# Performance work log

Hardware: AMD Instinct MI355X
Metric: run time of the kernel (lower is better)

## Reference

```python
import jax, jax.numpy as jnp
import numpy as np

L = 8          # fixed number of instance labels (0 = background), all assumed present
DV = 0.5       # delta_v
DD = 1.5       # delta_d
LOSS_WEIGHT = 1.0


def _safe_norm(x, axis):
    sq = jnp.sum(x * x, axis=axis)
    pos = sq > 0
    return jnp.sqrt(jnp.where(pos, sq, 1.0)) * pos.astype(x.dtype)


def _per_image(emb, inst, kern, tmask):
    # emb: [D,H,W], inst: [H,W] int, kern/tmask: [H,W] float
    D, H, W = emb.shape
    HW = H * W
    tm = (tmask > 0.5).astype(inst.dtype)
    kb = (kern > 0.5).astype(inst.dtype)
    inst = inst * tm
    inst_k = (inst * kb).reshape(-1)          # kernel-region labels
    inst_f = inst.reshape(-1)                 # full-region labels
    emb_f = emb.reshape(D, -1).T              # [HW, D]

    # --- generate_coef: first/second occurrence (row-major) of each label ---
    flat = jnp.arange(HW)
    eq = inst_f[None, :] == jnp.arange(L)[:, None]          # [L, HW]
    idxs = jnp.where(eq, flat[None, :], HW)
    first = jnp.min(idxs, axis=1)
    second = jnp.min(jnp.where(idxs == first[:, None], HW, idxs), axis=1)
    first = jnp.minimum(first, HW - 1)
    second = jnp.minimum(second, HW - 1)
    r0, c0 = first // W, first % W
    r1, c1 = second // W, second % W
    # pos_id = (tmp[0,0], tmp[1,0], tmp[0,-1], tmp[1,-1]) as in the source
    pos = jnp.stack([r0, r1, c0, c1], axis=1).astype(jnp.float32)  # [L,4]
    diag = jnp.sqrt(jnp.float32(H * H + W * W))
    coef_diag = jnp.exp(jnp.sqrt((pos[:, 0] - pos[:, 2]) ** 2 +
                                 (pos[:, 1] - pos[:, 3]) ** 2) / diag / 2.0)
    zmask = (jnp.arange(L) > 0).astype(jnp.float32)          # skip label 0
    coef_diag = coef_diag * zmask
    s = pos[:, 0] + pos[:, 2]
    t = pos[:, 1] + pos[:, 3]
    dp = jnp.sqrt((s[:, None] - s[None, :]) ** 2 + (t[:, None] - t[None, :]) ** 2)
    coef_off = 1.0 - 20.0 * jnp.exp(-4.0 - 2.5 * dp / diag)
    eye = jnp.eye(L, dtype=bool)
    coef = jnp.where(eye, coef_diag[:, None], coef_off)
    coef = coef * zmask[:, None] * zmask[None, :]

    # --- per-label kernel means (segment mean) ---
    ones = jnp.ones((HW,), jnp.float32)
    cnt_k = jax.ops.segment_sum(ones, inst_k, num_segments=L)
    mean = jax.ops.segment_sum(emb_f, inst_k, num_segments=L)
    mean = mean / jnp.maximum(cnt_k, 1.0)[:, None]           # [L, D]
    mean = mean * zmask[:, None]

    # --- l_agg: per-pixel distance to own-label mean, segment-mean per label ---
    mean_px = mean[inst_f]                                   # [HW, D] gather
    dist = _safe_norm(emb_f - mean_px, axis=1)
    cd_px = coef_diag[inst_f]
    val = jnp.log(jax.nn.relu(cd_px * dist - DV) ** 2 + 1.0)
    cnt = jax.ops.segment_sum(ones, inst_f, num_segments=L)
    l_agg_per = jax.ops.segment_sum(val, inst_f, num_segments=L) / jnp.maximum(cnt, 1.0)
    l_agg = jnp.mean(l_agg_per[1:])

    # --- l_dis: coefficient-weighted pairwise hinge between means ---
    Dn = _safe_norm(mean[:, None, :] - mean[None, :, :], axis=-1)  # [L, L]
    pm = (~eye) & (zmask[:, None] > 0) & (zmask[None, :] > 0)
    vals = jnp.log(jax.nn.relu(2.0 * DD - coef * Dn) ** 2 + 1.0)
    l_dis = jnp.sum(jnp.where(pm, vals, 0.0)) / ((L - 1) * (L - 2))

    # --- l_reg ---
    l_reg = jnp.mean(jnp.log(_safe_norm(mean, axis=1) + 1.0)) * 0.001
    return l_agg + l_dis + l_reg


def reference(emb, instance, kernel, training_mask, bboxes):
    # bboxes is accepted but unused, matching the original forward_single
    loss_batch = jax.vmap(_per_image)(emb, instance, kernel, training_mask)
    return LOSS_WEIGHT * jnp.mean(loss_batch)


def setup_inputs() -> dict:
    key = jax.random.key(0)
    k1, k2, k3, k4, k5 = jax.random.split(key, 5)
    B, D, H, W = 8, 4, 640, 640
    emb = jax.random.normal(k1, (B, D, H, W), dtype=jnp.float32)
    instance = jax.random.randint(k2, (B, H, W), 0, L, dtype=jnp.int32)
    kernel = jax.random.uniform(k3, (B, H, W), dtype=jnp.float32)
    training_mask = jax.random.uniform(k4, (B, H, W), dtype=jnp.float32)
    bboxes = jax.random.uniform(k5, (B, 10, 4), dtype=jnp.float32)
    return {"emb": emb, "instance": instance, "kernel": kernel,
            "training_mask": training_mask, "bboxes": bboxes}
```

## Files before the change

### kernel.cpp

```cpp
#include <hip/hip_runtime.h>
#include <hip/hip_bf16.h>

#define B_   8
#define D_   4
#define H_   640
#define W_   640
#define HW_  (H_ * W_)
#define L_   8
#define BLOCK 256
#define ITER  8


__device__ __forceinline__ void fatom_add(float* p, float v) {
    unsafeAtomicAdd(p, v);
}

__global__ void k_init(int* firstIdx, int* secondIdx, float* fbuf) {
    int t = threadIdx.x;
    if (t < B_ * L_) { firstIdx[t] = HW_; secondIdx[t] = HW_; }
    for (int i = t; i < 448; i += blockDim.x) fbuf[i] = 0.0f;
}

__global__ __launch_bounds__(BLOCK) void k_pass1(
        const float* __restrict__ emb, const int* __restrict__ inst,
        const float* __restrict__ kern, const float* __restrict__ tmask,
        int* __restrict__ firstIdx, float* __restrict__ cntk,
        float* __restrict__ cntf, float* __restrict__ sumemb) {
    __shared__ int   sFirst[L_];
    __shared__ float sCntK[L_], sCntF[L_];
    __shared__ float sSum[L_ * D_];

    const int tid = threadIdx.x;
    if (tid < L_) { sFirst[tid] = HW_; sCntK[tid] = 0.0f; sCntF[tid] = 0.0f; }
    if (tid < L_ * D_) sSum[tid] = 0.0f;
    __syncthreads();

    const int b    = blockIdx.y;
    const int base = b * HW_;

    #pragma unroll
    for (int it = 0; it < ITER; ++it) {
        int p = blockIdx.x * (BLOCK * ITER) + it * BLOCK + tid;
        int lab  = inst[base + p];
        float tm = tmask[base + p];
        int lf = (tm > 0.5f) ? lab : 0;
        if (lf > 0) {
            atomicMin(&sFirst[lf], p);
            fatom_add(&sCntF[lf], 1.0f);
            float kn = kern[base + p];
            if (kn > 0.5f) {
                fatom_add(&sCntK[lf], 1.0f);
                #pragma unroll
                for (int d = 0; d < D_; ++d)
                    fatom_add(&sSum[lf * D_ + d], emb[(b * D_ + d) * HW_ + p]);
            }
        }
    }
    __syncthreads();

    if (tid >= 1 && tid < L_) {
        atomicMin(&firstIdx[b * L_ + tid], sFirst[tid]);
        fatom_add(&cntf[b * L_ + tid], sCntF[tid]);
        fatom_add(&cntk[b * L_ + tid], sCntK[tid]);
    }
    if (tid >= D_ && tid < L_ * D_)
        fatom_add(&sumemb[b * L_ * D_ + tid], sSum[tid]);
}

__global__ __launch_bounds__(BLOCK) void k_pass2(
        const int* __restrict__ inst, const float* __restrict__ tmask,
        const int* __restrict__ firstIdx, int* __restrict__ secondIdx) {
    __shared__ int sFirst[L_];
    __shared__ int sSecond[L_];

    const int tid = threadIdx.x;
    const int b   = blockIdx.y;
    if (tid < L_) { sFirst[tid] = firstIdx[b * L_ + tid]; sSecond[tid] = HW_; }
    __syncthreads();

    const int base = b * HW_;
    #pragma unroll
    for (int it = 0; it < ITER; ++it) {
        int p = blockIdx.x * (BLOCK * ITER) + it * BLOCK + tid;
        int lab  = inst[base + p];
        float tm = tmask[base + p];
        int lf = (tm > 0.5f) ? lab : 0;
        if (lf > 0 && p != sFirst[lf]) atomicMin(&sSecond[lf], p);
    }
    __syncthreads();

    if (tid >= 1 && tid < L_)
        atomicMin(&secondIdx[b * L_ + tid], sSecond[tid]);
}

__global__ __launch_bounds__(BLOCK) void k_pass3(
        const float* __restrict__ emb, const int* __restrict__ inst,
        const float* __restrict__ tmask,
        const int* __restrict__ firstIdx, const int* __restrict__ secondIdx,
        const float* __restrict__ cntk, const float* __restrict__ sumemb,
        float* __restrict__ sumval) {
    __shared__ float sMean[L_ * D_];
    __shared__ float sCd[L_];
    __shared__ float sVal[L_];

    const int tid = threadIdx.x;
    const int b   = blockIdx.y;

    if (tid < L_ * D_) {
        int l = tid / D_;
        float c = fmaxf(cntk[b * L_ + l], 1.0f);
        sMean[tid] = (l > 0) ? sumemb[b * L_ * D_ + tid] / c : 0.0f;
    }
    if (tid < L_) {
        float cd = 0.0f;
        if (tid > 0) {
            const float diag = sqrtf((float)(H_ * H_ + W_ * W_));
            int f = min(firstIdx[b * L_ + tid],  HW_ - 1);
            int s = min(secondIdx[b * L_ + tid], HW_ - 1);
            float r0 = (float)(f / W_), c0 = (float)(f % W_);
            float r1 = (float)(s / W_), c1 = (float)(s % W_);
            cd = expf(sqrtf((r0 - c0) * (r0 - c0) + (r1 - c1) * (r1 - c1))
                      / diag * 0.5f);
        }
        sCd[tid]  = cd;
        sVal[tid] = 0.0f;
    }
    __syncthreads();

    const int base = b * HW_;
    #pragma unroll
    for (int it = 0; it < ITER; ++it) {
        int p = blockIdx.x * (BLOCK * ITER) + it * BLOCK + tid;
        int lab  = inst[base + p];
        float tm = tmask[base + p];
        int lf = (tm > 0.5f) ? lab : 0;
        if (lf > 0) {
            float d2 = 0.0f;
            #pragma unroll
            for (int d = 0; d < D_; ++d) {
                float e = emb[(b * D_ + d) * HW_ + p] - sMean[lf * D_ + d];
                d2 += e * e;
            }
            float dist = (d2 > 0.0f) ? sqrtf(d2) : 0.0f;
            float x = sCd[lf] * dist - 0.5f;
            if (x > 0.0f) fatom_add(&sVal[lf], logf(x * x + 1.0f));
        }
    }
    __syncthreads();

    if (tid >= 1 && tid < L_)
        fatom_add(&sumval[b * L_ + tid], sVal[tid]);
}

__global__ void k_final(const int* __restrict__ firstIdx,
                        const int* __restrict__ secondIdx,
                        const float* __restrict__ cntk,
                        const float* __restrict__ cntf,
                        const float* __restrict__ sumemb,
                        const float* __restrict__ sumval,
                        float* __restrict__ out) {
    __shared__ float sLoss[B_];
    const int b = threadIdx.x;
    if (b < B_) {
        const float diag = sqrtf((float)(H_ * H_ + W_ * W_));
        float mean[L_][D_];
        float ss[L_], tt[L_];
        #pragma unroll
        for (int l = 0; l < L_; ++l) {
            float c = fmaxf(cntk[b * L_ + l], 1.0f);
            #pragma unroll
            for (int d = 0; d < D_; ++d)
                mean[l][d] = (l > 0) ? sumemb[(b * L_ + l) * D_ + d] / c : 0.0f;
            int f = min(firstIdx[b * L_ + l],  HW_ - 1);
            int s = min(secondIdx[b * L_ + l], HW_ - 1);
            float r0 = (float)(f / W_), c0 = (float)(f % W_);
            float r1 = (float)(s / W_), c1 = (float)(s % W_);
            ss[l] = r0 + c0;
            tt[l] = r1 + c1;
        }
        float ldis = 0.0f;
        #pragma unroll
        for (int i = 1; i < L_; ++i) {
            #pragma unroll
            for (int j = 1; j < L_; ++j) {
                if (i == j) continue;
                float d2 = 0.0f;
                #pragma unroll
                for (int d = 0; d < D_; ++d) {
                    float df = mean[i][d] - mean[j][d];
                    d2 += df * df;
                }
                float Dn = (d2 > 0.0f) ? sqrtf(d2) : 0.0f;
                float dx = ss[i] - ss[j], dy = tt[i] - tt[j];
                float dp = sqrtf(dx * dx + dy * dy);
                float coef = 1.0f - 20.0f * expf(-4.0f - 2.5f * dp / diag);
                float x = 3.0f - coef * Dn;
                if (x > 0.0f) ldis += logf(x * x + 1.0f);
            }
        }
        ldis *= (1.0f / 42.0f);
        float lreg = 0.0f;
        #pragma unroll
        for (int l = 0; l < L_; ++l) {
            float d2 = 0.0f;
            #pragma unroll
            for (int d = 0; d < D_; ++d) d2 += mean[l][d] * mean[l][d];
            float n = (d2 > 0.0f) ? sqrtf(d2) : 0.0f;
            lreg += logf(n + 1.0f);
        }
        lreg = lreg * (1.0f / L_) * 0.001f;
        float lagg = 0.0f;
        #pragma unroll
        for (int l = 1; l < L_; ++l)
            lagg += sumval[b * L_ + l] / fmaxf(cntf[b * L_ + l], 1.0f);
        lagg *= (1.0f / (L_ - 1));
        sLoss[b] = lagg + ldis + lreg;
    }
    __syncthreads();
    if (threadIdx.x == 0) {
        float tot = 0.0f;
        #pragma unroll
        for (int i = 0; i < B_; ++i) tot += sLoss[i];
        out[0] = tot * (1.0f / B_);
    }
}

extern "C" void kernel_launch(void* const* d_in, const int* in_sizes, int n_in,
                              void* d_out, int out_size, void* d_ws, size_t ws_size,
                              hipStream_t stream) {
    const float* emb   = (const float*)d_in[0];
    const int*   inst  = (const int*)  d_in[1];
    const float* kern  = (const float*)d_in[2];
    const float* tmask = (const float*)d_in[3];

    int*   firstIdx  = (int*)d_ws;
    int*   secondIdx = firstIdx + B_ * L_;
    float* cntk      = (float*)(secondIdx + B_ * L_);
    float* cntf      = cntk + B_ * L_;
    float* sumemb    = cntf + B_ * L_;
    float* sumval    = sumemb + B_ * L_ * D_;
    float* out       = (float*)d_out;

    dim3 grid(HW_ / (BLOCK * ITER), B_);

    k_init <<<1, 256, 0, stream>>>(firstIdx, secondIdx, cntk);
    k_pass1<<<grid, BLOCK, 0, stream>>>(emb, inst, kern, tmask,
                                        firstIdx, cntk, cntf, sumemb);
    k_pass2<<<grid, BLOCK, 0, stream>>>(inst, tmask, firstIdx, secondIdx);
    k_pass3<<<grid, BLOCK, 0, stream>>>(emb, inst, tmask, firstIdx, secondIdx,
                                        cntk, sumemb, sumval);
    k_final<<<1, 64, 0, stream>>>(firstIdx, secondIdx, cntk, cntf,
                                  sumemb, sumval, out);
}
```

Before: 182.8 us.

## Fuse first/second index search into pass1 and replace LDS atomics with wave reductions

Pass1 now tracks the first and second occurrence of each label in per-thread registers and merges them with min/max wave shuffles, which removes the separate pass2 scan over inst and tmask. Per-pixel shared-memory atomics in pass1 and pass3 become per-thread per-label accumulators followed by wave shuffle reductions, with one atomic per wave. k_final is parallelised across 512 threads, one per (batch, i, j) pair. The cost is much higher register use from 7 labels times 7 accumulators per thread, plus unconditional emb loads and select arithmetic for every pixel.

Measured after the change: 172.8 us. -5.5%, faster.

```diff
diff --git a/kernel.cpp b/kernel.cpp
--- a/kernel.cpp
+++ b/kernel.cpp
@@ -7,11 +7,11 @@
 #define W_   640
 #define HW_  (H_ * W_)
 #define L_   8
+#define NL   (L_ - 1)
 #define BLOCK 256
 #define ITER  8
 
-
-__device__ __forceinline__ void fatom_add(float* p, float v) {
+__device__ __forceinline__ void gatom_add(float* p, float v) {
     unsafeAtomicAdd(p, v);
 }
 
@@ -24,73 +24,100 @@
 __global__ __launch_bounds__(BLOCK) void k_pass1(
         const float* __restrict__ emb, const int* __restrict__ inst,
         const float* __restrict__ kern, const float* __restrict__ tmask,
-        int* __restrict__ firstIdx, float* __restrict__ cntk,
-        float* __restrict__ cntf, float* __restrict__ sumemb) {
-    __shared__ int   sFirst[L_];
-    __shared__ float sCntK[L_], sCntF[L_];
-    __shared__ float sSum[L_ * D_];
+        int* __restrict__ firstIdx, int* __restrict__ secondIdx,
+        float* __restrict__ cntk, float* __restrict__ cntf,
+        float* __restrict__ sumemb) {
+    __shared__ float sCntF[L_], sCntK[L_], sSum[L_ * D_];
+    __shared__ int   sM1[L_], sM2[L_];
 
     const int tid = threadIdx.x;
-    if (tid < L_) { sFirst[tid] = HW_; sCntK[tid] = 0.0f; sCntF[tid] = 0.0f; }
-    if (tid < L_ * D_) sSum[tid] = 0.0f;
+    if (tid < L_) { sCntF[tid] = 0.f; sCntK[tid] = 0.f; sM1[tid] = HW_; sM2[tid] = HW_; }
+    if (tid < L_ * D_) sSum[tid] = 0.f;
     __syncthreads();
 
     const int b    = blockIdx.y;
     const int base = b * HW_;
+
+    float cf[NL], ck[NL], sm[NL][D_];
+    int   m1[NL], m2[NL];
+    #pragma unroll
+    for (int l = 0; l < NL; ++l) {
+        cf[l] = 0.f; ck[l] = 0.f; m1[l] = HW_; m2[l] = HW_;
+        #pragma unroll
+        for (int d = 0; d < D_; ++d) sm[l][d] = 0.f;
+    }
 
     #pragma unroll
     for (int it = 0; it < ITER; ++it) {
         int p = blockIdx.x * (BLOCK * ITER) + it * BLOCK + tid;
         int lab  = inst[base + p];
         float tm = tmask[base + p];
+        float kn = kern[base + p];
         int lf = (tm > 0.5f) ? lab : 0;
-        if (lf > 0) {
-            atomicMin(&sFirst[lf], p);
-            fatom_add(&sCntF[lf], 1.0f);
-            float kn = kern[base + p];
-            if (kn > 0.5f) {
-                fatom_add(&sCntK[lf], 1.0f);
-                #pragma unroll
-                for (int d = 0; d < D_; ++d)
-                    fatom_add(&sSum[lf * D_ + d], emb[(b * D_ + d) * HW_ + p]);
-            }
+        bool kb = (kn > 0.5f);
+        float e0 = emb[(b * D_ + 0) * HW_ + p];
+        float e1 = emb[(b * D_ + 1) * HW_ + p];
+        float e2 = emb[(b * D_ + 2) * HW_ + p];
+        float e3 = emb[(b * D_ + 3) * HW_ + p];
+
+        #pragma unroll
+        for (int l = 1; l < L_; ++l) {
+            const int k = l - 1;
+            bool pf = (lf == l);
+            cf[k] += pf ? 1.0f : 0.0f;
+            float mk = (pf && kb) ? 1.0f : 0.0f;
+            ck[k] += mk;
+            sm[k][0] += mk * e0;
+            sm[k][1] += mk * e1;
+            sm[k][2] += mk * e2;
+            sm[k][3] += mk * e3;
+            bool t1 = pf && (m1[k] == HW_);
+            bool t2 = pf && !t1 && (m2[k] == HW_);
+            m1[k] = t1 ? p : m1[k];
+            m2[k] = t2 ? p : m2[k];
+        }
+    }
+
+    #pragma unroll
+    for (int l = 0; l < NL; ++l) {
+        #pragma unroll
+        for (int off = 32; off > 0; off >>= 1) {
+            cf[l] += __shfl_down(cf[l], off);
+            ck[l] += __shfl_down(ck[l], off);
+            sm[l][0] += __shfl_down(sm[l][0], off);
+            sm[l][1] += __shfl_down(sm[l][1], off);
+            sm[l][2] += __shfl_down(sm[l][2], off);
+            sm[l][3] += __shfl_down(sm[l][3], off);
+            int o1 = __shfl_down(m1[l], off);
+            int o2 = __shfl_down(m2[l], off);
+            m2[l] = min(min(m2[l], o2), max(m1[l], o1));
+            m1[l] = min(m1[l], o1);
+        }
+    }
+
+    if ((tid & 63) == 0) {
+        #pragma unroll
+        for (int l = 0; l < NL; ++l) {
+            atomicAdd(&sCntF[l + 1], cf[l]);
+            atomicAdd(&sCntK[l + 1], ck[l]);
+            #pragma unroll
+            for (int d = 0; d < D_; ++d) atomicAdd(&sSum[(l + 1) * D_ + d], sm[l][d]);
+            int old = atomicMin(&sM1[l + 1], m1[l]);
+            atomicMin(&sM2[l + 1], max(old, m1[l]));
+            atomicMin(&sM2[l + 1], m2[l]);
         }
     }
     __syncthreads();
 
     if (tid >= 1 && tid < L_) {
-        atomicMin(&firstIdx[b * L_ + tid], sFirst[tid]);
-        fatom_add(&cntf[b * L_ + tid], sCntF[tid]);
-        fatom_add(&cntk[b * L_ + tid], sCntK[tid]);
+        gatom_add(&cntf[b * L_ + tid], sCntF[tid]);
+        gatom_add(&cntk[b * L_ + tid], sCntK[tid]);
+        int old = atomicMin(&firstIdx[b * L_ + tid], sM1[tid]);
+        atomicMin(&secondIdx[b * L_ + tid], max(old, sM1[tid]));
+        atomicMin(&secondIdx[b * L_ + tid], sM2[tid]);
     }
     if (tid >= D_ && tid < L_ * D_)
-        fatom_add(&sumemb[b * L_ * D_ + tid], sSum[tid]);
-}
-
-__global__ __launch_bounds__(BLOCK) void k_pass2(
-        const int* __restrict__ inst, const float* __restrict__ tmask,
-        const int* __restrict__ firstIdx, int* __restrict__ secondIdx) {
-    __shared__ int sFirst[L_];
-    __shared__ int sSecond[L_];
-
-    const int tid = threadIdx.x;
-    const int b   = blockIdx.y;
-    if (tid < L_) { sFirst[tid] = firstIdx[b * L_ + tid]; sSecond[tid] = HW_; }
-    __syncthreads();
-
-    const int base = b * HW_;
-    #pragma unroll
-    for (int it = 0; it < ITER; ++it) {
-        int p = blockIdx.x * (BLOCK * ITER) + it * BLOCK + tid;
-        int lab  = inst[base + p];
-        float tm = tmask[base + p];
-        int lf = (tm > 0.5f) ? lab : 0;
-        if (lf > 0 && p != sFirst[lf]) atomicMin(&sSecond[lf], p);
-    }
-    __syncthreads();
-
-    if (tid >= 1 && tid < L_)
-        atomicMin(&secondIdx[b * L_ + tid], sSecond[tid]);
+        gatom_add(&sumemb[b * L_ * D_ + tid], sSum[tid]);
 }
 
 __global__ __launch_bounds__(BLOCK) void k_pass3(
@@ -128,100 +155,111 @@
     __syncthreads();
 
     const int base = b * HW_;
+    float vs[NL];
+    #pragma unroll
+    for (int l = 0; l < NL; ++l) vs[l] = 0.f;
+
     #pragma unroll
     for (int it = 0; it < ITER; ++it) {
         int p = blockIdx.x * (BLOCK * ITER) + it * BLOCK + tid;
         int lab  = inst[base + p];
         float tm = tmask[base + p];
         int lf = (tm > 0.5f) ? lab : 0;
-        if (lf > 0) {
-            float d2 = 0.0f;
-            #pragma unroll
-            for (int d = 0; d < D_; ++d) {
-                float e = emb[(b * D_ + d) * HW_ + p] - sMean[lf * D_ + d];
-                d2 += e * e;
-            }
-            float dist = (d2 > 0.0f) ? sqrtf(d2) : 0.0f;
-            float x = sCd[lf] * dist - 0.5f;
-            if (x > 0.0f) fatom_add(&sVal[lf], logf(x * x + 1.0f));
-        }
+        float d2 = 0.0f;
+        #pragma unroll
+        for (int d = 0; d < D_; ++d) {
+            float e = emb[(b * D_ + d) * HW_ + p] - sMean[lf * D_ + d];
+            d2 += e * e;
+        }
+        float dist = sqrtf(d2);
+        float x = fmaxf(sCd[lf] * dist - 0.5f, 0.0f);
+        float val = logf(x * x + 1.0f);
+        #pragma unroll
+        for (int l = 1; l < L_; ++l)
+            vs[l - 1] += (lf == l) ? val : 0.0f;
+    }
+
+    #pragma unroll
+    for (int l = 0; l < NL; ++l) {
+        #pragma unroll
+        for (int off = 32; off > 0; off >>= 1)
+            vs[l] += __shfl_down(vs[l], off);
+    }
+    if ((tid & 63) == 0) {
+        #pragma unroll
+        for (int l = 0; l < NL; ++l) atomicAdd(&sVal[l + 1], vs[l]);
     }
     __syncthreads();
 
     if (tid >= 1 && tid < L_)
-        fatom_add(&sumval[b * L_ + tid], sVal[tid]);
-}
-
-__global__ void k_final(const int* __restrict__ firstIdx,
-                        const int* __restrict__ secondIdx,
-                        const float* __restrict__ cntk,
-                        const float* __restrict__ cntf,
-                        const float* __restrict__ sumemb,
-                        const float* __restrict__ sumval,
-                        float* __restrict__ out) {
-    __shared__ float sLoss[B_];
-    const int b = threadIdx.x;
-    if (b < B_) {
-        const float diag = sqrtf((float)(H_ * H_ + W_ * W_));
-        float mean[L_][D_];
-        float ss[L_], tt[L_];
-        #pragma unroll
-        for (int l = 0; l < L_; ++l) {
-            float c = fmaxf(cntk[b * L_ + l], 1.0f);
-            #pragma unroll
-            for (int d = 0; d < D_; ++d)
-                mean[l][d] = (l > 0) ? sumemb[(b * L_ + l) * D_ + d] / c : 0.0f;
-            int f = min(firstIdx[b * L_ + l],  HW_ - 1);
-            int s = min(secondIdx[b * L_ + l], HW_ - 1);
-            float r0 = (float)(f / W_), c0 = (float)(f % W_);
-            float r1 = (float)(s / W_), c1 = (float)(s % W_);
-            ss[l] = r0 + c0;
-            tt[l] = r1 + c1;
-        }
-        float ldis = 0.0f;
-        #pragma unroll
-        for (int i = 1; i < L_; ++i) {
-            #pragma unroll
-            for (int j = 1; j < L_; ++j) {
-                if (i == j) continue;
-                float d2 = 0.0f;
-                #pragma unroll
-                for (int d = 0; d < D_; ++d) {
-                    float df = mean[i][d] - mean[j][d];
-                    d2 += df * df;
-                }
-                float Dn = (d2 > 0.0f) ? sqrtf(d2) : 0.0f;
-                float dx = ss[i] - ss[j], dy = tt[i] - tt[j];
-                float dp = sqrtf(dx * dx + dy * dy);
-                float coef = 1.0f - 20.0f * expf(-4.0f - 2.5f * dp / diag);
-                float x = 3.0f - coef * Dn;
-                if (x > 0.0f) ldis += logf(x * x + 1.0f);
-            }
-        }
-        ldis *= (1.0f / 42.0f);
-        float lreg = 0.0f;
-        #pragma unroll
-        for (int l = 0; l < L_; ++l) {
-            float d2 = 0.0f;
-            #pragma unroll
-            for (int d = 0; d < D_; ++d) d2 += mean[l][d] * mean[l][d];
-            float n = (d2 > 0.0f) ? sqrtf(d2) : 0.0f;
-            lreg += logf(n + 1.0f);
-        }
-        lreg = lreg * (1.0f / L_) * 0.001f;
-        float lagg = 0.0f;
-        #pragma unroll
-        for (int l = 1; l < L_; ++l)
-            lagg += sumval[b * L_ + l] / fmaxf(cntf[b * L_ + l], 1.0f);
-        lagg *= (1.0f / (L_ - 1));
-        sLoss[b] = lagg + ldis + lreg;
-    }
-    __syncthreads();
-    if (threadIdx.x == 0) {
-        float tot = 0.0f;
-        #pragma unroll
-        for (int i = 0; i < B_; ++i) tot += sLoss[i];
-        out[0] = tot * (1.0f / B_);
+        gatom_add(&sumval[b * L_ + tid], sVal[tid]);
+}
+
+__global__ __launch_bounds__(512) void k_final(
+        const int* __restrict__ firstIdx, const int* __restrict__ secondIdx,
+        const float* __restrict__ cntk, const float* __restrict__ cntf,
+        const float* __restrict__ sumemb, const float* __restrict__ sumval,
+        float* __restrict__ out) {
+    __shared__ float sWave[8];
+    const int tid = threadIdx.x;
+    const int b = tid >> 6, ij = tid & 63, i = ij >> 3, j = ij & 7;
+    const float diag = sqrtf((float)(H_ * H_ + W_ * W_));
+
+    float mi[D_], mj[D_];
+    {
+        float ci = fmaxf(cntk[b * L_ + i], 1.0f);
+        float cj = fmaxf(cntk[b * L_ + j], 1.0f);
+        #pragma unroll
+        for (int d = 0; d < D_; ++d) {
+            mi[d] = (i > 0) ? sumemb[(b * L_ + i) * D_ + d] / ci : 0.0f;
+            mj[d] = (j > 0) ? sumemb[(b * L_ + j) * D_ + d] / cj : 0.0f;
+        }
+    }
+
+    float contrib = 0.0f;
+    if (j == 0) {
+        float d2 = 0.f;
+        #pragma unroll
+        for (int d = 0; d < D_; ++d) d2 += mi[d] * mi[d];
+        float n = (d2 > 0.f) ? sqrtf(d2) : 0.f;
+        contrib += logf(n + 1.0f) * (0.001f / (float)L_);
+    }
+    if (i == 0 && j >= 1) {
+        contrib += sumval[b * L_ + j] / fmaxf(cntf[b * L_ + j], 1.0f) * (1.0f / (float)NL);
+    }
+    if (i >= 1 && j >= 1 && i != j) {
+        float d2 = 0.f;
+        #pragma unroll
+        for (int d = 0; d < D_; ++d) {
+            float df = mi[d] - mj[d];
+            d2 += df * df;
+        }
+        float Dn = (d2 > 0.f) ? sqrtf(d2) : 0.f;
+        int fi = min(firstIdx[b * L_ + i],  HW_ - 1);
+        int si = min(secondIdx[b * L_ + i], HW_ - 1);
+        int fj = min(firstIdx[b * L_ + j],  HW_ - 1);
+        int sj = min(secondIdx[b * L_ + j], HW_ - 1);
+        float ssi = (float)(fi / W_) + (float)(fi % W_);
+        float tti = (float)(si / W_) + (float)(si % W_);
+        float ssj = (float)(fj / W_) + (float)(fj % W_);
+        float ttj = (float)(sj / W_) + (float)(sj % W_);
+        float dx = ssi - ssj, dy = tti - ttj;
+        float dp = sqrtf(dx * dx + dy * dy);
+        float coef = 1.0f - 20.0f * expf(-4.0f - 2.5f * dp / diag);
+        float x = fmaxf(3.0f - coef * Dn, 0.0f);
+        contrib += logf(x * x + 1.0f) * (1.0f / 42.0f);
+    }
+
+    #pragma unroll
+    for (int off = 32; off > 0; off >>= 1)
+        contrib += __shfl_down(contrib, off);
+    if ((tid & 63) == 0) sWave[tid >> 6] = contrib;
+    __syncthreads();
+    if (tid == 0) {
+        float t = 0.f;
+        #pragma unroll
+        for (int w = 0; w < 8; ++w) t += sWave[w];
+        out[0] = t * (1.0f / (float)B_);
     }
 }
 
@@ -245,10 +283,9 @@
 
     k_init <<<1, 256, 0, stream>>>(firstIdx, secondIdx, cntk);
     k_pass1<<<grid, BLOCK, 0, stream>>>(emb, inst, kern, tmask,
-                                        firstIdx, cntk, cntf, sumemb);
-    k_pass2<<<grid, BLOCK, 0, stream>>>(inst, tmask, firstIdx, secondIdx);
+                                        firstIdx, secondIdx, cntk, cntf, sumemb);
     k_pass3<<<grid, BLOCK, 0, stream>>>(emb, inst, tmask, firstIdx, secondIdx,
                                         cntk, sumemb, sumval);
-    k_final<<<1, 64, 0, stream>>>(firstIdx, secondIdx, cntk, cntf,
-                                  sumemb, sumval, out);
-}
+    k_final<<<1, 512, 0, stream>>>(firstIdx, secondIdx, cntk, cntf,
+                                   sumemb, sumval, out);
+}
```
